# Kernel optimization log

Hardware: AMD Instinct MI355X
Metric: run time of the kernel (lower is better)

The kernel has to match this reference:

```python
import jax, jax.numpy as jnp
import numpy as np

EPS = 1e-9


def setup_inputs() -> dict:
    key = jax.random.key(0)
    kE, kQ, kK, kV = jax.random.split(key, 4)
    B, S, D = 8, 2048, 256
    return {
        "E": jax.random.normal(kE, (B, S, D), dtype=jnp.float32),
        "WQ": jax.random.normal(kQ, (D, D), dtype=jnp.float32) * (1.0 / np.sqrt(D)),
        "WK": jax.random.normal(kK, (D, D), dtype=jnp.float32) * (1.0 / np.sqrt(D)),
        "WV": jax.random.normal(kV, (D, D), dtype=jnp.float32) * (1.0 / np.sqrt(D)),
    }


def reference(E, WQ, WK, WV):
    # E: [B, S, D]; WQ/WK/WV: [D, D] (torch Linear weight, applied as x @ W.T)
    D = E.shape[-1]
    scale = jnp.asarray(np.sqrt(D), dtype=E.dtype)
    Q = jnp.einsum('bsd,ed->bse', E, WQ)
    K = jnp.einsum('bsd,ed->bse', E, WK)
    V = jnp.einsum('bsd,ed->bse', E, WV)
    # Full score matrix [B, S, S] (non-flash, as in the original)
    W = jnp.einsum('bqd,bkd->bqk', Q, K) / scale
    # mask=True path: causal tril mask, additionally zeroed where W == 0 exactly
    S_len = W.shape[-1]
    tril = jnp.tril(jnp.ones((S_len, S_len), dtype=W.dtype))  # [S, S]
    M = jnp.where(W == 0, jnp.zeros_like(W), tril[None, :, :])
    # custom masked softmax with epsilon denominator
    x_max = jnp.max(W, axis=-1, keepdims=True)
    x_exp = jnp.exp(W - x_max) * M
    A = x_exp / (jnp.sum(x_exp, axis=-1, keepdims=True) + EPS)
    return jnp.einsum('bqk,bkd->bqd', A, V)
```

## Files before the change

### kernel.cpp

```cpp
#include <hip/hip_runtime.h>
#include <stdint.h>


typedef __attribute__((ext_vector_type(8)))  short bf16x8;
typedef __attribute__((ext_vector_type(4)))  float f32x4;
typedef __attribute__((ext_vector_type(16))) float f32x16;

#define NEGF  -3.0e38f
#define MINIT -1.0e30f

__device__ __forceinline__ unsigned short f2bf(float f){
  union { float f; unsigned u; } v; v.f = f;
  unsigned r = v.u + 0x7FFFu + ((v.u >> 16) & 1u);
  return (unsigned short)(r >> 16);
}
__device__ __forceinline__ unsigned pk2(float a, float b){
  return (unsigned)f2bf(a) | ((unsigned)f2bf(b) << 16);
}
__device__ __forceinline__ float bf2f(unsigned short h){
  union { unsigned u; float f; } v; v.u = ((unsigned)h) << 16; return v.f;
}

__global__ void wconv_kernel(const float* __restrict__ WQ, const float* __restrict__ WK,
                             const float* __restrict__ WV, unsigned short* __restrict__ Wb)
{
  const int widx = blockIdx.x, kk = blockIdx.y, n = threadIdx.x;
  const float* W = (widx==0) ? WQ : ((widx==1) ? WK : WV);
  unsigned short* dst = Wb + (size_t)widx*65536 + kk*8192 + n*32;
#pragma unroll
  for (int gp=0; gp<4; ++gp){
    const int g = gp ^ (n & 3);
    const float* src = W + (size_t)n*256 + kk*32 + g*8;
    float4 a = *reinterpret_cast<const float4*>(src);
    float4 c = *reinterpret_cast<const float4*>(src + 4);
    uint4 v; v.x = pk2(a.x,a.y); v.y = pk2(a.z,a.w); v.z = pk2(c.x,c.y); v.w = pk2(c.z,c.w);
    *reinterpret_cast<uint4*>(dst + gp*8) = v;
  }
}

__global__ __launch_bounds__(256, 3) void qkv_proj_kernel(
    const float* __restrict__ E, const unsigned short* __restrict__ Wb,
    unsigned short* __restrict__ Qb, unsigned short* __restrict__ Ka,
    unsigned short* __restrict__ Vf)
{
  __shared__ unsigned short As[32*256];
  __shared__ unsigned short Bs[2][8192];

  const int m0 = blockIdx.x * 32;
  const int b  = m0 >> 11;
  const int sb = m0 & 2047;
  const int t = threadIdx.x, lane = t & 63, w = t >> 6;
  const int hi = lane >> 4, lo = lane & 15;

  auto stageB = [&](int widx, int kk, int buf){
    const char* src = (const char*)Wb + widx*131072 + kk*16384;
    char* dst = (char*)Bs[buf];
#pragma unroll
    for (int c=0;c<4;c++){
      const int off = c*4096 + t*16;
      __builtin_amdgcn_global_load_lds(
        (const __attribute__((address_space(1))) unsigned int*)(src + off),
        (__attribute__((address_space(3))) unsigned int*)(dst + off), 16, 0, 0);
    }
  };

  stageB(0, 0, 0);
  {
    const int r = t >> 3, c0 = (t & 7) * 32;
    const float* ga = E + (size_t)(m0 + r)*256 + c0;
#pragma unroll
    for (int gg=0; gg<4; ++gg){
      float4 x = *reinterpret_cast<const float4*>(ga + gg*8);
      float4 y = *reinterpret_cast<const float4*>(ga + gg*8 + 4);
      uint4 v; v.x = pk2(x.x,x.y); v.y = pk2(x.z,x.w); v.z = pk2(y.x,y.y); v.w = pk2(y.z,y.w);
      const int g = (t & 7)*4 + gg;
      *reinterpret_cast<uint4*>((char*)As + r*512 + ((g ^ (r & 7)) << 4)) = v;
    }
  }

  const f32x4 fzero = {0.f,0.f,0.f,0.f};
  const int u = sb >> 5;
  for (int widx=0; widx<3; ++widx){
    f32x4 acc[2][4];
#pragma unroll
    for (int mi=0;mi<2;mi++)
#pragma unroll
      for (int f=0;f<4;f++) acc[mi][f] = fzero;
    if (widx) stageB(widx, 0, 0);

    for (int kk=0; kk<8; ++kk){
      const int bb = kk & 1;
      if (kk < 7) stageB(widx, kk+1, bb^1);
      if (kk < 7) asm volatile("s_waitcnt vmcnt(4) lgkmcnt(0)" ::: "memory");
      else        asm volatile("s_waitcnt vmcnt(0) lgkmcnt(0)" ::: "memory");
      __builtin_amdgcn_sched_barrier(0);
      __builtin_amdgcn_s_barrier();
      __builtin_amdgcn_sched_barrier(0);

      bf16x8 afr[2], bfr[4];
#pragma unroll
      for (int mi=0;mi<2;mi++){
        const int r = mi*16 + lo;
        afr[mi] = *reinterpret_cast<const bf16x8*>(
            (const char*)As + r*512 + (((kk*4 + hi) ^ (r & 7)) << 4));
      }
#pragma unroll
      for (int f=0;f<4;f++){
        const int n = w*64 + f*16 + lo;
        bfr[f] = *reinterpret_cast<const bf16x8*>(
            (const char*)Bs[bb] + n*64 + ((hi ^ (n & 3)) << 4));
      }
#pragma unroll
      for (int mi=0;mi<2;mi++)
#pragma unroll
        for (int f=0;f<4;f++)
          acc[mi][f] = __builtin_amdgcn_mfma_f32_16x16x32_bf16(afr[mi], bfr[f], acc[mi][f], 0,0,0);

      asm volatile("s_waitcnt lgkmcnt(0)" ::: "memory");
      __builtin_amdgcn_sched_barrier(0);
      __builtin_amdgcn_s_barrier();
    }

    if (widx == 0){
#pragma unroll
      for (int mi=0;mi<2;mi++)
#pragma unroll
        for (int f=0;f<4;f++){
          const int col = w*64 + f*16 + lo;
#pragma unroll
          for (int r=0;r<4;r++)
            Qb[(size_t)(m0 + mi*16 + hi*4 + r)*256 + col] = f2bf(acc[mi][f][r]*0.0625f);
        }
    } else if (widx == 1){
      unsigned short* Kab = Ka + (size_t)b*524288 + (size_t)u*8192;
#pragma unroll
      for (int mi=0;mi<2;mi++)
#pragma unroll
        for (int f=0;f<4;f++){
          const int c = w*4 + f;
          const int j = lo & 7;
          const int lb = 32*(lo>>3) + mi*16 + hi*4;
#pragma unroll
          for (int r=0;r<4;r++)
            Kab[(size_t)(c*64 + lb + r)*8 + j] = f2bf(acc[mi][f][r]);
        }
    } else {
      unsigned short* Vfb = Vf + (size_t)b*524288;
#pragma unroll
      for (int mi=0;mi<2;mi++)
#pragma unroll
        for (int f=0;f<4;f++){
          const int d  = w*64 + f*16 + lo;
          const int dt = d >> 5;
          const int l  = 32*(hi&1) + (d&31);
          const int j0 = 4*(hi>>1);
          unsigned short* vp = Vfb + ((size_t)((u*2 + mi)*8 + dt)*64 + l)*8 + j0;
          uint2 pw; pw.x = pk2(acc[mi][f][0], acc[mi][f][1]);
          pw.y = pk2(acc[mi][f][2], acc[mi][f][3]);
          *reinterpret_cast<uint2*>(vp) = pw;
        }
    }
  }
}

__global__ __launch_bounds__(256, 2) void attn_kernel(
    const unsigned short* __restrict__ Qb, const unsigned short* __restrict__ Ka,
    const unsigned short* __restrict__ Vf, float* __restrict__ Out,
    const int sched, unsigned short* __restrict__ Pb, float* __restrict__ ML)
{
  __shared__ char Lds[2][32768];

  const int bid  = blockIdx.x;
  const int b    = bid & 7;
  const int slot = bid >> 3;
  int tau, chunk, mode, u0, u1;
  if (sched){
    tau = 31 - (slot >> 1); chunk = slot & 1;
    u0 = chunk ? (tau + 1) : 0;
    u1 = chunk ? (2*tau + 2) : (tau + 1);
    mode = 1 + chunk;
  } else {
    tau = 31 - slot; chunk = 0; u0 = 0; u1 = 2*tau + 2; mode = 0;
  }
  const int Qbase = tau * 64;

  const int t = threadIdx.x;
  const int lane = t & 63, w = t >> 6;
  const int qs = w >> 1, dh = w & 1;
  const int l31 = lane & 31, h5 = lane >> 5;
  const int q_l = Qbase + qs*32 + l31;
  const int diagu = 2*tau + qs;

  const char* Kab = (const char*)Ka + (size_t)b*1048576;
  const char* Vfb = (const char*)Vf + (size_t)b*1048576;

  auto stage = [&](int uu, int buf){
    const char* gk = Kab + (size_t)uu*16384;
    const char* gv = Vfb + (size_t)uu*16384;
    char* lk = Lds[buf];
    char* lv = Lds[buf] + 16384;
#pragma unroll
    for (int i=0;i<4;i++){
      const int off = i*4096 + t*16;
      __builtin_amdgcn_global_load_lds(
        (const __attribute__((address_space(1))) unsigned int*)(gk + off),
        (__attribute__((address_space(3))) unsigned int*)(lk + off), 16, 0, 0);
      __builtin_amdgcn_global_load_lds(
        (const __attribute__((address_space(1))) unsigned int*)(gv + off),
        (__attribute__((address_space(3))) unsigned int*)(lv + off), 16, 0, 0);
    }
  };

  bf16x8 qf[16];
  {
    const unsigned short* Qp = Qb + ((size_t)(b*2048 + q_l))*256 + h5*8;
#pragma unroll
    for (int c=0;c<16;c++) qf[c] = *reinterpret_cast<const bf16x8*>(Qp + c*16);
  }

  const f32x16 z16 = {0.f,0.f,0.f,0.f,0.f,0.f,0.f,0.f,0.f,0.f,0.f,0.f,0.f,0.f,0.f,0.f};
  f32x16 accO[4];
#pragma unroll
  for (int i=0;i<4;i++) accO[i] = z16;
  float m_run = MINIT, l_run = 0.f;

  stage(u0, 0);
  if (u0 + 1 < u1) stage(u0 + 1, 1);

  for (int u = u0; u < u1; ++u){
    const int buf = (u - u0) & 1;
    if (u + 1 < u1) asm volatile("s_waitcnt vmcnt(8)" ::: "memory");
    else            asm volatile("s_waitcnt vmcnt(0)" ::: "memory");
    __builtin_amdgcn_sched_barrier(0);
    __builtin_amdgcn_s_barrier();
    __builtin_amdgcn_sched_barrier(0);

    const char* kt = Lds[buf];
    const char* lv = Lds[buf] + 16384 + dh*4096 + lane*16;

    f32x16 sv0 = z16, sv1 = z16;
#pragma unroll
    for (int c=0;c<16;c+=2){
      bf16x8 a0 = *reinterpret_cast<const bf16x8*>(kt + c*1024 + lane*16);
      bf16x8 a1 = *reinterpret_cast<const bf16x8*>(kt + (c+1)*1024 + lane*16);
      sv0 = __builtin_amdgcn_mfma_f32_32x32x16_bf16(a0, qf[c],   sv0, 0,0,0);
      sv1 = __builtin_amdgcn_mfma_f32_32x32x16_bf16(a1, qf[c+1], sv1, 0,0,0);
    }
    f32x16 s16 = sv0 + sv1;

    bf16x8 vf0[4], vf1[4];
#pragma unroll
    for (int i=0;i<4;i++){
      vf0[i] = *reinterpret_cast<const bf16x8*>(lv + i*1024);
      vf1[i] = *reinterpret_cast<const bf16x8*>(lv + 8192 + i*1024);
    }

    if (u >= diagu){
      const int kvb = u*32 + 4*h5;
#pragma unroll
      for (int r=0;r<16;r++){
        const int kv = kvb + (r&3) + 8*(r>>2);
        if (kv > q_l) s16[r] = NEGF;
      }
    }

    float t8[8], t4[4];
#pragma unroll
    for (int i=0;i<8;i++) t8[i] = fmaxf(s16[i], s16[i+8]);
#pragma unroll
    for (int i=0;i<4;i++) t4[i] = fmaxf(t8[i], t8[i+4]);
    float pmax = fmaxf(fmaxf(t4[0],t4[1]), fmaxf(t4[2],t4[3]));
    pmax = fmaxf(pmax, __shfl_xor(pmax, 32, 64));

    if (!__all(pmax - m_run <= 8.0f)){
      const float mn = fmaxf(m_run, pmax);
      const float alpha = __expf(m_run - mn);
#pragma unroll
      for (int i=0;i<4;i++) accO[i] *= alpha;
      l_run *= alpha;
      m_run = mn;
    }
    float p[16];
#pragma unroll
    for (int r=0;r<16;r++) p[r] = __expf(s16[r] - m_run);
#pragma unroll
    for (int i=0;i<8;i++) t8[i] = p[i] + p[i+8];
#pragma unroll
    for (int i=0;i<4;i++) t4[i] = t8[i] + t8[i+4];
    float ls = (t4[0]+t4[1]) + (t4[2]+t4[3]);
    ls += __shfl_xor(ls, 32, 64);
    l_run += ls;

    union { bf16x8 v; unsigned u32[4]; } pa0, pa1;
#pragma unroll
    for (int k=0;k<4;k++){
      pa0.u32[k] = pk2(p[2*k],   p[2*k+1]);
      pa1.u32[k] = pk2(p[8+2*k], p[9+2*k]);
    }

#pragma unroll
    for (int i=0;i<4;i++){
      accO[i] = __builtin_amdgcn_mfma_f32_32x32x16_bf16(vf0[i], pa0.v, accO[i], 0,0,0);
      accO[i] = __builtin_amdgcn_mfma_f32_32x32x16_bf16(vf1[i], pa1.v, accO[i], 0,0,0);
    }

    asm volatile("s_waitcnt lgkmcnt(0)" ::: "memory");
    __builtin_amdgcn_sched_barrier(0);
    __builtin_amdgcn_s_barrier();
    if (u + 2 < u1) stage(u + 2, buf);
  }

  if (mode && dh == 0 && lane < 32){
    float* mlp = ML + ((size_t)(((b*32 + tau)*2 + chunk)*64 + qs*32 + lane))*2;
    mlp[0] = m_run; mlp[1] = l_run;
  }

  const float inv = (mode == 0) ? 1.0f/(l_run + 1e-9f) : 1.0f;
  float* Tw = (float*)(&Lds[0][0]) + w*2048;
  const int qloc = lane >> 1, dc = (lane & 1) * 16;
#pragma unroll
  for (int i=0;i<4;i++){
#pragma unroll
    for (int r=0;r<16;r++)
      Tw[l31*33 + ((r&3) + 8*(r>>2) + 4*h5)] = accO[i][r] * inv;
    asm volatile("s_waitcnt lgkmcnt(0)" ::: "memory");
    __builtin_amdgcn_sched_barrier(0);
    const float* srcT = &Tw[qloc*33 + dc];
    if (mode < 2){
      float* dst = Out + ((size_t)(b*2048 + Qbase + qs*32 + qloc))*256 + dh*128 + i*32 + dc;
#pragma unroll
      for (int k=0;k<4;k++){
        float4 vv = { srcT[4*k], srcT[4*k+1], srcT[4*k+2], srcT[4*k+3] };
        *reinterpret_cast<float4*>(dst + 4*k) = vv;
      }
    } else {
      unsigned short* pb = Pb + (((size_t)(b*32 + tau)*64 + qs*32 + qloc))*256
                              + dh*128 + i*32 + dc;
      uint4 w0, w1;
      w0.x = pk2(srcT[0],  srcT[1]);  w0.y = pk2(srcT[2],  srcT[3]);
      w0.z = pk2(srcT[4],  srcT[5]);  w0.w = pk2(srcT[6],  srcT[7]);
      w1.x = pk2(srcT[8],  srcT[9]);  w1.y = pk2(srcT[10], srcT[11]);
      w1.z = pk2(srcT[12], srcT[13]); w1.w = pk2(srcT[14], srcT[15]);
      *reinterpret_cast<uint4*>(pb)     = w0;
      *reinterpret_cast<uint4*>(pb + 8) = w1;
    }
    asm volatile("s_waitcnt lgkmcnt(0)" ::: "memory");
    __builtin_amdgcn_sched_barrier(0);
  }
}

__global__ void combine_kernel(float* __restrict__ Out, const unsigned short* __restrict__ Pb,
                               const float* __restrict__ ML)
{
  const int b = blockIdx.x & 7, tt = blockIdx.x >> 3;
  const int t = threadIdx.x;
  const int q = t >> 2, dg = (t & 3) * 64;
  const float* mlp = ML + ((size_t)((b*32 + tt)*2)*64)*2;
  const float m0 = mlp[q*2],            l0 = mlp[q*2 + 1];
  const float m1 = mlp[(64 + q)*2],     l1 = mlp[(64 + q)*2 + 1];
  const float M  = fmaxf(m0, m1);
  const float e0 = __expf(m0 - M), e1 = __expf(m1 - M);
  const float inv = 1.0f/(e0*l0 + e1*l1 + 1e-9f);
  float* O = Out + ((size_t)(b*2048 + tt*64 + q))*256 + dg;
  const unsigned short* P = Pb + ((size_t)((b*32 + tt)*64 + q))*256 + dg;
#pragma unroll
  for (int k=0;k<8;k++){
    float4 a0 = *reinterpret_cast<const float4*>(O + 8*k);
    float4 a1 = *reinterpret_cast<const float4*>(O + 8*k + 4);
    uint4 pv = *reinterpret_cast<const uint4*>(P + 8*k);
    const unsigned short* us = (const unsigned short*)&pv;
    float4 o0, o1;
    o0.x = (e0*a0.x + e1*bf2f(us[0]))*inv; o0.y = (e0*a0.y + e1*bf2f(us[1]))*inv;
    o0.z = (e0*a0.z + e1*bf2f(us[2]))*inv; o0.w = (e0*a0.w + e1*bf2f(us[3]))*inv;
    o1.x = (e0*a1.x + e1*bf2f(us[4]))*inv; o1.y = (e0*a1.y + e1*bf2f(us[5]))*inv;
    o1.z = (e0*a1.z + e1*bf2f(us[6]))*inv; o1.w = (e0*a1.w + e1*bf2f(us[7]))*inv;
    *reinterpret_cast<float4*>(O + 8*k)     = o0;
    *reinterpret_cast<float4*>(O + 8*k + 4) = o1;
  }
}

extern "C" void kernel_launch(void* const* d_in, const int* in_sizes, int n_in,
                              void* d_out, int out_size, void* d_ws, size_t ws_size,
                              hipStream_t stream)
{
  const float* E  = (const float*)d_in[0];
  const float* WQ = (const float*)d_in[1];
  const float* WK = (const float*)d_in[2];
  const float* WV = (const float*)d_in[3];
  const size_t elems = (size_t)8*2048*256;

  unsigned short* Qb = (unsigned short*)d_ws;
  unsigned short* Ka = Qb + elems;
  unsigned short* Vf = Ka + elems;
  unsigned short* Wb = Vf + elems;
  const size_t base = 3*elems*2 + 393216;

  const size_t PB = (size_t)8*32*64*256*2;
  const size_t MLSZ = (size_t)8*32*2*64*2*4;
  if (ws_size < base) return;
  const int sched = (ws_size >= base + PB + MLSZ) ? 1 : 0;
  unsigned short* Pb = (unsigned short*)((char*)d_ws + base);
  float* ML = (float*)((char*)d_ws + base + PB);

  wconv_kernel<<<dim3(3,8), 256, 0, stream>>>(WQ, WK, WV, Wb);
  qkv_proj_kernel<<<512, 256, 0, stream>>>(E, Wb, Qb, Ka, Vf);
  attn_kernel<<<sched ? 512 : 256, 256, 0, stream>>>(Qb, Ka, Vf, (float*)d_out, sched, Pb, ML);
  if (sched) combine_kernel<<<256, 256, 0, stream>>>((float*)d_out, Pb, ML);
}
```

Measured before the change: 89.19 us.

## Split attention KV range into up to four balanced chunks, halve projection tiles

The attention kernel now splits each query tile's causal KV range into 1, 2 or 4 balanced chunks, depending on workspace size, and interleaves long and short tiles in launch order. Partial results are merged by a generalized combine kernel. V fragments are read straight from global memory instead of being staged in LDS, which halves LDS use and lets the kernel raise its occupancy target to four blocks. The projection kernel uses 16-row tiles to double the grid, and output stores become nontemporal. These changes aim to improve load balance and occupancy, at the cost of more partial-buffer traffic and uncached V loads.

```diff
diff --git a/kernel.cpp b/kernel.cpp
--- a/kernel.cpp
+++ b/kernel.cpp
@@ -5,6 +5,7 @@
 typedef __attribute__((ext_vector_type(8)))  short bf16x8;
 typedef __attribute__((ext_vector_type(4)))  float f32x4;
 typedef __attribute__((ext_vector_type(16))) float f32x16;
+typedef __attribute__((ext_vector_type(4)))  unsigned int u32x4;
 
 #define NEGF  -3.0e38f
 #define MINIT -1.0e30f
@@ -19,6 +20,12 @@
 }
 __device__ __forceinline__ float bf2f(unsigned short h){
   union { unsigned u; float f; } v; v.u = ((unsigned)h) << 16; return v.f;
+}
+__device__ __forceinline__ void nt_store4f(float* p, f32x4 v){
+  __builtin_nontemporal_store(v, (f32x4*)p);
+}
+__device__ __forceinline__ void nt_store4u(unsigned short* p, u32x4 v){
+  __builtin_nontemporal_store(v, (u32x4*)p);
 }
 
 __global__ void wconv_kernel(const float* __restrict__ WQ, const float* __restrict__ WK,
@@ -38,17 +45,19 @@
   }
 }
 
-__global__ __launch_bounds__(256, 3) void qkv_proj_kernel(
+__global__ __launch_bounds__(256, 4) void qkv_proj_kernel(
     const float* __restrict__ E, const unsigned short* __restrict__ Wb,
     unsigned short* __restrict__ Qb, unsigned short* __restrict__ Ka,
     unsigned short* __restrict__ Vf)
 {
-  __shared__ unsigned short As[32*256];
+  __shared__ unsigned short As[16*256];
   __shared__ unsigned short Bs[2][8192];
 
-  const int m0 = blockIdx.x * 32;
+  const int m0 = blockIdx.x * 16;
   const int b  = m0 >> 11;
   const int sb = m0 & 2047;
+  const int u  = sb >> 5;
+  const int h  = (sb >> 4) & 1;
   const int t = threadIdx.x, lane = t & 63, w = t >> 6;
   const int hi = lane >> 4, lo = lane & 15;
 
@@ -66,26 +75,23 @@
 
   stageB(0, 0, 0);
   {
-    const int r = t >> 3, c0 = (t & 7) * 32;
-    const float* ga = E + (size_t)(m0 + r)*256 + c0;
-#pragma unroll
-    for (int gg=0; gg<4; ++gg){
+    const int r = t >> 4, cg = t & 15;
+    const float* ga = E + (size_t)(m0 + r)*256 + cg*16;
+#pragma unroll
+    for (int gg=0; gg<2; ++gg){
       float4 x = *reinterpret_cast<const float4*>(ga + gg*8);
       float4 y = *reinterpret_cast<const float4*>(ga + gg*8 + 4);
       uint4 v; v.x = pk2(x.x,x.y); v.y = pk2(x.z,x.w); v.z = pk2(y.x,y.y); v.w = pk2(y.z,y.w);
-      const int g = (t & 7)*4 + gg;
+      const int g = cg*2 + gg;
       *reinterpret_cast<uint4*>((char*)As + r*512 + ((g ^ (r & 7)) << 4)) = v;
     }
   }
 
   const f32x4 fzero = {0.f,0.f,0.f,0.f};
-  const int u = sb >> 5;
   for (int widx=0; widx<3; ++widx){
-    f32x4 acc[2][4];
-#pragma unroll
-    for (int mi=0;mi<2;mi++)
-#pragma unroll
-      for (int f=0;f<4;f++) acc[mi][f] = fzero;
+    f32x4 acc[4];
+#pragma unroll
+    for (int f=0;f<4;f++) acc[f] = fzero;
     if (widx) stageB(widx, 0, 0);
 
     for (int kk=0; kk<8; ++kk){
@@ -97,13 +103,9 @@
       __builtin_amdgcn_s_barrier();
       __builtin_amdgcn_sched_barrier(0);
 
-      bf16x8 afr[2], bfr[4];
-#pragma unroll
-      for (int mi=0;mi<2;mi++){
-        const int r = mi*16 + lo;
-        afr[mi] = *reinterpret_cast<const bf16x8*>(
-            (const char*)As + r*512 + (((kk*4 + hi) ^ (r & 7)) << 4));
-      }
+      bf16x8 afr = *reinterpret_cast<const bf16x8*>(
+          (const char*)As + lo*512 + (((kk*4 + hi) ^ (lo & 7)) << 4));
+      bf16x8 bfr[4];
 #pragma unroll
       for (int f=0;f<4;f++){
         const int n = w*64 + f*16 + lo;
@@ -111,10 +113,8 @@
             (const char*)Bs[bb] + n*64 + ((hi ^ (n & 3)) << 4));
       }
 #pragma unroll
-      for (int mi=0;mi<2;mi++)
-#pragma unroll
-        for (int f=0;f<4;f++)
-          acc[mi][f] = __builtin_amdgcn_mfma_f32_16x16x32_bf16(afr[mi], bfr[f], acc[mi][f], 0,0,0);
+      for (int f=0;f<4;f++)
+        acc[f] = __builtin_amdgcn_mfma_f32_16x16x32_bf16(afr, bfr[f], acc[f], 0,0,0);
 
       asm volatile("s_waitcnt lgkmcnt(0)" ::: "memory");
       __builtin_amdgcn_sched_barrier(0);
@@ -123,65 +123,57 @@
 
     if (widx == 0){
 #pragma unroll
-      for (int mi=0;mi<2;mi++)
-#pragma unroll
-        for (int f=0;f<4;f++){
-          const int col = w*64 + f*16 + lo;
-#pragma unroll
-          for (int r=0;r<4;r++)
-            Qb[(size_t)(m0 + mi*16 + hi*4 + r)*256 + col] = f2bf(acc[mi][f][r]*0.0625f);
-        }
+      for (int f=0;f<4;f++){
+        const int col = w*64 + f*16 + lo;
+#pragma unroll
+        for (int r=0;r<4;r++)
+          Qb[(size_t)(m0 + hi*4 + r)*256 + col] = f2bf(acc[f][r]*0.0625f);
+      }
     } else if (widx == 1){
       unsigned short* Kab = Ka + (size_t)b*524288 + (size_t)u*8192;
 #pragma unroll
-      for (int mi=0;mi<2;mi++)
-#pragma unroll
-        for (int f=0;f<4;f++){
-          const int c = w*4 + f;
-          const int j = lo & 7;
-          const int lb = 32*(lo>>3) + mi*16 + hi*4;
-#pragma unroll
-          for (int r=0;r<4;r++)
-            Kab[(size_t)(c*64 + lb + r)*8 + j] = f2bf(acc[mi][f][r]);
-        }
+      for (int f=0;f<4;f++){
+        const int c = w*4 + f;
+        const int j = lo & 7;
+        const int lb = 32*(lo>>3) + h*16 + hi*4;
+#pragma unroll
+        for (int r=0;r<4;r++)
+          Kab[(size_t)(c*64 + lb + r)*8 + j] = f2bf(acc[f][r]);
+      }
     } else {
       unsigned short* Vfb = Vf + (size_t)b*524288;
 #pragma unroll
-      for (int mi=0;mi<2;mi++)
-#pragma unroll
-        for (int f=0;f<4;f++){
-          const int d  = w*64 + f*16 + lo;
-          const int dt = d >> 5;
-          const int l  = 32*(hi&1) + (d&31);
-          const int j0 = 4*(hi>>1);
-          unsigned short* vp = Vfb + ((size_t)((u*2 + mi)*8 + dt)*64 + l)*8 + j0;
-          uint2 pw; pw.x = pk2(acc[mi][f][0], acc[mi][f][1]);
-          pw.y = pk2(acc[mi][f][2], acc[mi][f][3]);
-          *reinterpret_cast<uint2*>(vp) = pw;
-        }
-    }
-  }
-}
-
-__global__ __launch_bounds__(256, 2) void attn_kernel(
+      for (int f=0;f<4;f++){
+        const int d  = w*64 + f*16 + lo;
+        const int dt = d >> 5;
+        const int l  = 32*(hi&1) + (d&31);
+        const int j0 = 4*(hi>>1);
+        unsigned short* vp = Vfb + ((size_t)((u*2 + h)*8 + dt)*64 + l)*8 + j0;
+        uint2 pw; pw.x = pk2(acc[f][0], acc[f][1]);
+        pw.y = pk2(acc[f][2], acc[f][3]);
+        *reinterpret_cast<uint2*>(vp) = pw;
+      }
+    }
+  }
+}
+
+__global__ __launch_bounds__(256, 4) void attn_kernel(
     const unsigned short* __restrict__ Qb, const unsigned short* __restrict__ Ka,
     const unsigned short* __restrict__ Vf, float* __restrict__ Out,
-    const int sched, unsigned short* __restrict__ Pb, float* __restrict__ ML)
+    const int shift, unsigned short* __restrict__ Pb, float* __restrict__ ML)
 {
-  __shared__ char Lds[2][32768];
-
-  const int bid  = blockIdx.x;
-  const int b    = bid & 7;
-  const int slot = bid >> 3;
-  int tau, chunk, mode, u0, u1;
-  if (sched){
-    tau = 31 - (slot >> 1); chunk = slot & 1;
-    u0 = chunk ? (tau + 1) : 0;
-    u1 = chunk ? (2*tau + 2) : (tau + 1);
-    mode = 1 + chunk;
-  } else {
-    tau = 31 - slot; chunk = 0; u0 = 0; u1 = 2*tau + 2; mode = 0;
-  }
+  __shared__ char Kt[2][16384];
+
+  const int nch = 1 << shift;
+  const int bid = blockIdx.x, b = bid & 7, slot = bid >> 3;
+  const int ts = slot >> shift, chunk = slot & (nch - 1);
+  const int tau = (ts < 16) ? (31 - ts) : (ts - 16);
+  const int len = 2*tau + 2;
+  const int qq = len >> shift, rem = len & (nch - 1);
+  const int u0 = chunk*qq + ((chunk < rem) ? chunk : rem);
+  const int u1 = u0 + qq + ((chunk < rem) ? 1 : 0);
+  const int mode = (nch == 1) ? 0 : ((chunk == 0) ? 1 : 2);
+  const int psl = nch - 1;
   const int Qbase = tau * 64;
 
   const int t = threadIdx.x;
@@ -195,19 +187,14 @@
   const char* Vfb = (const char*)Vf + (size_t)b*1048576;
 
   auto stage = [&](int uu, int buf){
-    const char* gk = Kab + (size_t)uu*16384;
-    const char* gv = Vfb + (size_t)uu*16384;
-    char* lk = Lds[buf];
-    char* lv = Lds[buf] + 16384;
+    const char* src = Kab + (size_t)uu*16384;
+    char* dstl = (char*)Kt[buf];
 #pragma unroll
     for (int i=0;i<4;i++){
       const int off = i*4096 + t*16;
       __builtin_amdgcn_global_load_lds(
-        (const __attribute__((address_space(1))) unsigned int*)(gk + off),
-        (__attribute__((address_space(3))) unsigned int*)(lk + off), 16, 0, 0);
-      __builtin_amdgcn_global_load_lds(
-        (const __attribute__((address_space(1))) unsigned int*)(gv + off),
-        (__attribute__((address_space(3))) unsigned int*)(lv + off), 16, 0, 0);
+        (const __attribute__((address_space(1))) unsigned int*)(src + off),
+        (__attribute__((address_space(3))) unsigned int*)(dstl + off), 16, 0, 0);
     }
   };
 
@@ -224,99 +211,100 @@
   for (int i=0;i<4;i++) accO[i] = z16;
   float m_run = MINIT, l_run = 0.f;
 
-  stage(u0, 0);
-  if (u0 + 1 < u1) stage(u0 + 1, 1);
-
-  for (int u = u0; u < u1; ++u){
-    const int buf = (u - u0) & 1;
-    if (u + 1 < u1) asm volatile("s_waitcnt vmcnt(8)" ::: "memory");
-    else            asm volatile("s_waitcnt vmcnt(0)" ::: "memory");
-    __builtin_amdgcn_sched_barrier(0);
-    __builtin_amdgcn_s_barrier();
-    __builtin_amdgcn_sched_barrier(0);
-
-    const char* kt = Lds[buf];
-    const char* lv = Lds[buf] + 16384 + dh*4096 + lane*16;
-
-    f32x16 sv0 = z16, sv1 = z16;
-#pragma unroll
-    for (int c=0;c<16;c+=2){
-      bf16x8 a0 = *reinterpret_cast<const bf16x8*>(kt + c*1024 + lane*16);
-      bf16x8 a1 = *reinterpret_cast<const bf16x8*>(kt + (c+1)*1024 + lane*16);
-      sv0 = __builtin_amdgcn_mfma_f32_32x32x16_bf16(a0, qf[c],   sv0, 0,0,0);
-      sv1 = __builtin_amdgcn_mfma_f32_32x32x16_bf16(a1, qf[c+1], sv1, 0,0,0);
-    }
-    f32x16 s16 = sv0 + sv1;
-
-    bf16x8 vf0[4], vf1[4];
-#pragma unroll
-    for (int i=0;i<4;i++){
-      vf0[i] = *reinterpret_cast<const bf16x8*>(lv + i*1024);
-      vf1[i] = *reinterpret_cast<const bf16x8*>(lv + 8192 + i*1024);
-    }
-
-    if (u >= diagu){
-      const int kvb = u*32 + 4*h5;
-#pragma unroll
-      for (int r=0;r<16;r++){
-        const int kv = kvb + (r&3) + 8*(r>>2);
-        if (kv > q_l) s16[r] = NEGF;
-      }
-    }
-
-    float t8[8], t4[4];
-#pragma unroll
-    for (int i=0;i<8;i++) t8[i] = fmaxf(s16[i], s16[i+8]);
-#pragma unroll
-    for (int i=0;i<4;i++) t4[i] = fmaxf(t8[i], t8[i+4]);
-    float pmax = fmaxf(fmaxf(t4[0],t4[1]), fmaxf(t4[2],t4[3]));
-    pmax = fmaxf(pmax, __shfl_xor(pmax, 32, 64));
-
-    if (!__all(pmax - m_run <= 8.0f)){
-      const float mn = fmaxf(m_run, pmax);
-      const float alpha = __expf(m_run - mn);
-#pragma unroll
-      for (int i=0;i<4;i++) accO[i] *= alpha;
-      l_run *= alpha;
-      m_run = mn;
-    }
-    float p[16];
-#pragma unroll
-    for (int r=0;r<16;r++) p[r] = __expf(s16[r] - m_run);
-#pragma unroll
-    for (int i=0;i<8;i++) t8[i] = p[i] + p[i+8];
-#pragma unroll
-    for (int i=0;i<4;i++) t4[i] = t8[i] + t8[i+4];
-    float ls = (t4[0]+t4[1]) + (t4[2]+t4[3]);
-    ls += __shfl_xor(ls, 32, 64);
-    l_run += ls;
-
-    union { bf16x8 v; unsigned u32[4]; } pa0, pa1;
-#pragma unroll
-    for (int k=0;k<4;k++){
-      pa0.u32[k] = pk2(p[2*k],   p[2*k+1]);
-      pa1.u32[k] = pk2(p[8+2*k], p[9+2*k]);
-    }
-
-#pragma unroll
-    for (int i=0;i<4;i++){
-      accO[i] = __builtin_amdgcn_mfma_f32_32x32x16_bf16(vf0[i], pa0.v, accO[i], 0,0,0);
-      accO[i] = __builtin_amdgcn_mfma_f32_32x32x16_bf16(vf1[i], pa1.v, accO[i], 0,0,0);
-    }
-
-    asm volatile("s_waitcnt lgkmcnt(0)" ::: "memory");
-    __builtin_amdgcn_sched_barrier(0);
-    __builtin_amdgcn_s_barrier();
-    if (u + 2 < u1) stage(u + 2, buf);
+  if (u0 < u1){
+    stage(u0, 0);
+    if (u0 + 1 < u1) stage(u0 + 1, 1);
+
+    for (int u = u0; u < u1; ++u){
+      const int buf = (u - u0) & 1;
+      if (u + 1 < u1) asm volatile("s_waitcnt vmcnt(4)" ::: "memory");
+      else            asm volatile("s_waitcnt vmcnt(0)" ::: "memory");
+      __builtin_amdgcn_sched_barrier(0);
+      __builtin_amdgcn_s_barrier();
+      __builtin_amdgcn_sched_barrier(0);
+
+      const char* Vu = Vfb + (size_t)u*16384 + dh*4096 + lane*16;
+      bf16x8 vf0[4], vf1[4];
+#pragma unroll
+      for (int i=0;i<4;i++){
+        vf0[i] = *reinterpret_cast<const bf16x8*>(Vu + i*1024);
+        vf1[i] = *reinterpret_cast<const bf16x8*>(Vu + 8192 + i*1024);
+      }
+
+      const char* kt = Kt[buf];
+      f32x16 sv0 = z16, sv1 = z16;
+#pragma unroll
+      for (int c=0;c<16;c+=2){
+        bf16x8 a0 = *reinterpret_cast<const bf16x8*>(kt + c*1024 + lane*16);
+        bf16x8 a1 = *reinterpret_cast<const bf16x8*>(kt + (c+1)*1024 + lane*16);
+        sv0 = __builtin_amdgcn_mfma_f32_32x32x16_bf16(a0, qf[c],   sv0, 0,0,0);
+        sv1 = __builtin_amdgcn_mfma_f32_32x32x16_bf16(a1, qf[c+1], sv1, 0,0,0);
+      }
+      f32x16 s16 = sv0 + sv1;
+
+      asm volatile("s_waitcnt lgkmcnt(0)" ::: "memory");
+      __builtin_amdgcn_sched_barrier(0);
+      __builtin_amdgcn_s_barrier();
+      if (u + 2 < u1) stage(u + 2, buf);
+
+      if (u >= diagu){
+        const int kvb = u*32 + 4*h5;
+#pragma unroll
+        for (int r=0;r<16;r++){
+          const int kv = kvb + (r&3) + 8*(r>>2);
+          if (kv > q_l) s16[r] = NEGF;
+        }
+      }
+
+      float t8[8], t4[4];
+#pragma unroll
+      for (int i=0;i<8;i++) t8[i] = fmaxf(s16[i], s16[i+8]);
+#pragma unroll
+      for (int i=0;i<4;i++) t4[i] = fmaxf(t8[i], t8[i+4]);
+      float pmax = fmaxf(fmaxf(t4[0],t4[1]), fmaxf(t4[2],t4[3]));
+      pmax = fmaxf(pmax, __shfl_xor(pmax, 32, 64));
+
+      if (!__all(pmax - m_run <= 8.0f)){
+        const float mn = fmaxf(m_run, pmax);
+        const float alpha = __expf(m_run - mn);
+#pragma unroll
+        for (int i=0;i<4;i++) accO[i] *= alpha;
+        l_run *= alpha;
+        m_run = mn;
+      }
+      float p[16];
+#pragma unroll
+      for (int r=0;r<16;r++) p[r] = __expf(s16[r] - m_run);
+#pragma unroll
+      for (int i=0;i<8;i++) t8[i] = p[i] + p[i+8];
+#pragma unroll
+      for (int i=0;i<4;i++) t4[i] = t8[i] + t8[i+4];
+      float ls = (t4[0]+t4[1]) + (t4[2]+t4[3]);
+      ls += __shfl_xor(ls, 32, 64);
+      l_run += ls;
+
+      union { bf16x8 v; unsigned u32[4]; } pa0, pa1;
+#pragma unroll
+      for (int k=0;k<4;k++){
+        pa0.u32[k] = pk2(p[2*k],   p[2*k+1]);
+        pa1.u32[k] = pk2(p[8+2*k], p[9+2*k]);
+      }
+
+#pragma unroll
+      for (int i=0;i<4;i++){
+        accO[i] = __builtin_amdgcn_mfma_f32_32x32x16_bf16(vf0[i], pa0.v, accO[i], 0,0,0);
+        accO[i] = __builtin_amdgcn_mfma_f32_32x32x16_bf16(vf1[i], pa1.v, accO[i], 0,0,0);
+      }
+    }
   }
 
   if (mode && dh == 0 && lane < 32){
-    float* mlp = ML + ((size_t)(((b*32 + tau)*2 + chunk)*64 + qs*32 + lane))*2;
+    float* mlp = ML + ((size_t)((b*32 + tau)*nch + chunk)*64 + qs*32 + lane)*2;
     mlp[0] = m_run; mlp[1] = l_run;
   }
 
   const float inv = (mode == 0) ? 1.0f/(l_run + 1e-9f) : 1.0f;
-  float* Tw = (float*)(&Lds[0][0]) + w*2048;
+  float* Tw = (float*)(&Kt[0][0]) + w*2048;
   const int qloc = lane >> 1, dc = (lane & 1) * 16;
 #pragma unroll
   for (int i=0;i<4;i++){
@@ -326,23 +314,23 @@
     asm volatile("s_waitcnt lgkmcnt(0)" ::: "memory");
     __builtin_amdgcn_sched_barrier(0);
     const float* srcT = &Tw[qloc*33 + dc];
-    if (mode < 2){
+    if (mode <= 1){
       float* dst = Out + ((size_t)(b*2048 + Qbase + qs*32 + qloc))*256 + dh*128 + i*32 + dc;
 #pragma unroll
       for (int k=0;k<4;k++){
-        float4 vv = { srcT[4*k], srcT[4*k+1], srcT[4*k+2], srcT[4*k+3] };
-        *reinterpret_cast<float4*>(dst + 4*k) = vv;
+        f32x4 vv = { srcT[4*k], srcT[4*k+1], srcT[4*k+2], srcT[4*k+3] };
+        nt_store4f(dst + 4*k, vv);
       }
     } else {
-      unsigned short* pb = Pb + (((size_t)(b*32 + tau)*64 + qs*32 + qloc))*256
+      unsigned short* pb = Pb + ((size_t)((b*32 + tau)*psl + (chunk-1))*64 + qs*32 + qloc)*256
                               + dh*128 + i*32 + dc;
-      uint4 w0, w1;
+      u32x4 w0, w1;
       w0.x = pk2(srcT[0],  srcT[1]);  w0.y = pk2(srcT[2],  srcT[3]);
       w0.z = pk2(srcT[4],  srcT[5]);  w0.w = pk2(srcT[6],  srcT[7]);
       w1.x = pk2(srcT[8],  srcT[9]);  w1.y = pk2(srcT[10], srcT[11]);
       w1.z = pk2(srcT[12], srcT[13]); w1.w = pk2(srcT[14], srcT[15]);
-      *reinterpret_cast<uint4*>(pb)     = w0;
-      *reinterpret_cast<uint4*>(pb + 8) = w1;
+      nt_store4u(pb, w0);
+      nt_store4u(pb + 8, w1);
     }
     asm volatile("s_waitcnt lgkmcnt(0)" ::: "memory");
     __builtin_amdgcn_sched_barrier(0);
@@ -350,32 +338,53 @@
 }
 
 __global__ void combine_kernel(float* __restrict__ Out, const unsigned short* __restrict__ Pb,
-                               const float* __restrict__ ML)
+                               const float* __restrict__ ML, const int shift)
 {
+  const int nch = 1 << shift, psl = nch - 1;
   const int b = blockIdx.x & 7, tt = blockIdx.x >> 3;
   const int t = threadIdx.x;
   const int q = t >> 2, dg = (t & 3) * 64;
-  const float* mlp = ML + ((size_t)((b*32 + tt)*2)*64)*2;
-  const float m0 = mlp[q*2],            l0 = mlp[q*2 + 1];
-  const float m1 = mlp[(64 + q)*2],     l1 = mlp[(64 + q)*2 + 1];
-  const float M  = fmaxf(m0, m1);
-  const float e0 = __expf(m0 - M), e1 = __expf(m1 - M);
-  const float inv = 1.0f/(e0*l0 + e1*l1 + 1e-9f);
+
+  float mc[4], lc[4];
+#pragma unroll
+  for (int c=0;c<4;c++){
+    if (c < nch){
+      const float* mlp = ML + ((size_t)((b*32 + tt)*nch + c)*64 + q)*2;
+      mc[c] = mlp[0]; lc[c] = mlp[1];
+    } else { mc[c] = MINIT; lc[c] = 0.f; }
+  }
+  float M = fmaxf(fmaxf(mc[0],mc[1]), fmaxf(mc[2],mc[3]));
+  float e[4], L = 0.f;
+#pragma unroll
+  for (int c=0;c<4;c++){ e[c] = __expf(mc[c] - M); L += e[c]*lc[c]; }
+  const float inv = 1.0f/(L + 1e-9f);
+
   float* O = Out + ((size_t)(b*2048 + tt*64 + q))*256 + dg;
-  const unsigned short* P = Pb + ((size_t)((b*32 + tt)*64 + q))*256 + dg;
-#pragma unroll
-  for (int k=0;k<8;k++){
-    float4 a0 = *reinterpret_cast<const float4*>(O + 8*k);
-    float4 a1 = *reinterpret_cast<const float4*>(O + 8*k + 4);
-    uint4 pv = *reinterpret_cast<const uint4*>(P + 8*k);
-    const unsigned short* us = (const unsigned short*)&pv;
-    float4 o0, o1;
-    o0.x = (e0*a0.x + e1*bf2f(us[0]))*inv; o0.y = (e0*a0.y + e1*bf2f(us[1]))*inv;
-    o0.z = (e0*a0.z + e1*bf2f(us[2]))*inv; o0.w = (e0*a0.w + e1*bf2f(us[3]))*inv;
-    o1.x = (e0*a1.x + e1*bf2f(us[4]))*inv; o1.y = (e0*a1.y + e1*bf2f(us[5]))*inv;
-    o1.z = (e0*a1.z + e1*bf2f(us[6]))*inv; o1.w = (e0*a1.w + e1*bf2f(us[7]))*inv;
-    *reinterpret_cast<float4*>(O + 8*k)     = o0;
-    *reinterpret_cast<float4*>(O + 8*k + 4) = o1;
+  f32x4 acc[16];
+#pragma unroll
+  for (int k=0;k<16;k++){
+    f32x4 v = *reinterpret_cast<const f32x4*>(O + 4*k);
+    acc[k] = v * e[0];
+  }
+#pragma unroll
+  for (int c=1;c<4;c++){
+    if (c < nch){
+      const unsigned short* P = Pb + ((size_t)((b*32 + tt)*psl + (c-1))*64 + q)*256 + dg;
+#pragma unroll
+      for (int k=0;k<8;k++){
+        u32x4 pv = *reinterpret_cast<const u32x4*>(P + 8*k);
+        const unsigned short* us = (const unsigned short*)&pv;
+#pragma unroll
+        for (int j=0;j<4;j++) acc[2*k][j]   += e[c]*bf2f(us[j]);
+#pragma unroll
+        for (int j=0;j<4;j++) acc[2*k+1][j] += e[c]*bf2f(us[4+j]);
+      }
+    }
+  }
+#pragma unroll
+  for (int k=0;k<16;k++){
+    f32x4 v = acc[k] * inv;
+    *reinterpret_cast<f32x4*>(O + 4*k) = v;
   }
 }
 
@@ -395,15 +404,17 @@
   unsigned short* Wb = Vf + elems;
   const size_t base = 3*elems*2 + 393216;
 
-  const size_t PB = (size_t)8*32*64*256*2;
-  const size_t MLSZ = (size_t)8*32*2*64*2*4;
+  const size_t MLSZ = (size_t)8*32*4*64*2*4;
+  const size_t PB1  = (size_t)8*32*64*256*2;
   if (ws_size < base) return;
-  const int sched = (ws_size >= base + PB + MLSZ) ? 1 : 0;
-  unsigned short* Pb = (unsigned short*)((char*)d_ws + base);
-  float* ML = (float*)((char*)d_ws + base + PB);
+  int shift = 0;
+  if      (ws_size >= base + MLSZ + 3*PB1) shift = 2;
+  else if (ws_size >= base + MLSZ + 1*PB1) shift = 1;
+  float* ML = (float*)((char*)d_ws + base);
+  unsigned short* Pb = (unsigned short*)((char*)d_ws + base + MLSZ);
 
   wconv_kernel<<<dim3(3,8), 256, 0, stream>>>(WQ, WK, WV, Wb);
-  qkv_proj_kernel<<<512, 256, 0, stream>>>(E, Wb, Qb, Ka, Vf);
-  attn_kernel<<<sched ? 512 : 256, 256, 0, stream>>>(Qb, Ka, Vf, (float*)d_out, sched, Pb, ML);
-  if (sched) combine_kernel<<<256, 256, 0, stream>>>((float*)d_out, Pb, ML);
-}
+  qkv_proj_kernel<<<1024, 256, 0, stream>>>(E, Wb, Qb, Ka, Vf);
+  attn_kernel<<<256 << shift, 256, 0, stream>>>(Qb, Ka, Vf, (float*)d_out, shift, Pb, ML);
+  if (shift) combine_kernel<<<256, 256, 0, stream>>>((float*)d_out, Pb, ML, shift);
+}
```

Result: slower. 270.5 us (+203.3%).
